# Kernel optimization log

Hardware: AMD Instinct MI355X
Metric: run time of the kernel (lower is better)

Reference implementation:

```python
import jax, jax.numpy as jnp
import numpy as np

T, B, E, H, V, L = 128, 64, 1024, 1024, 10000, 2


def setup_inputs() -> dict:
    key = jax.random.key(0)
    ks = jax.random.split(key, 10)
    k = 1.0 / np.sqrt(H)
    u = lambda kk, shape, a: jax.random.uniform(kk, shape, jnp.float32, -a, a)
    return {
        "emb_table": u(ks[0], (V, E), 0.1),
        "W_in0": u(ks[1], (H, E), k),   # first layer input weight (no bias in linear_W)
        "Wh0": u(ks[2], (H, H), k),
        "b0": u(ks[3], (H,), k),
        "W_in1": u(ks[4], (H, H), k),
        "Wh1": u(ks[5], (H, H), k),
        "b1": u(ks[6], (H,), k),
        "Wdec": u(ks[7], (V, H), 0.1),
        "bdec": jnp.zeros((V,), jnp.float32),
        "hidden": jnp.zeros((L, B, H), jnp.float32),
        "tokens": jax.random.randint(ks[8], (T, B), 0, V, jnp.int32),
    }


def reference(emb_table, W_in0, Wh0, b0, W_in1, Wh1, b1, Wdec, bdec, hidden, tokens):
    # dp_keep_prob = 1.0 -> dropout is identity
    x_emb = emb_table[tokens]  # [T, B, E]

    def step(h, x):
        # h: [L, B, H]; x: [B, E]
        h0 = jnp.tanh(x @ W_in0.T + h[0] @ Wh0.T + b0)
        h1 = jnp.tanh(h0 @ W_in1.T + h[1] @ Wh1.T + b1)
        logits_t = h1 @ Wdec.T + bdec  # [B, V]
        return jnp.stack([h0, h1]), logits_t

    h_final, logits = jax.lax.scan(step, hidden, x_emb)
    return logits, h_final  # [T, B, V], [L, B, H]
```

## Files before the change

### kernel.cpp

```cpp
#include <hip/hip_runtime.h>
#include <hip/hip_bf16.h>
#include <stdint.h>

typedef __bf16 bf16_t;
typedef __bf16 bf16x8 __attribute__((ext_vector_type(8)));
typedef __bf16 bf16x4 __attribute__((ext_vector_type(4)));
typedef float  floatx4 __attribute__((ext_vector_type(4)));

#define T_STEPS 128
#define BATCH   64
#define EDIM    1024
#define HDIM    1024
#define VOCAB   10000
#define MROWS   (T_STEPS * BATCH)
#define RNN_BLOCKS 128
#define DEC_BLOCKS 128
#define BH      (BATCH * HDIM)
#define FSTRIDE 16
#define VTILES  79
#define NUNITS  (64 * VTILES)

__device__ __forceinline__ floatx4 mfma16(bf16x8 a, bf16x8 b, floatx4 c) {
    return __builtin_amdgcn_mfma_f32_16x16x32_bf16(a, b, c, 0, 0, 0);
}

__device__ __forceinline__ void gl_lds16(const bf16_t* g, bf16_t* l) {
    __builtin_amdgcn_global_load_lds(
        (const __attribute__((address_space(1))) void*)g,
        (__attribute__((address_space(3))) void*)l, 16, 0, 0);
}

__device__ __forceinline__ void store_bf16_bypass(bf16_t* p, float v) {
    union { bf16_t b; unsigned short u; } cv;
    cv.b = (bf16_t)v;
    unsigned int d = cv.u;
    asm volatile("global_store_short %0, %1, off sc0 sc1"
                 :: "v"(p), "v"(d) : "memory");
}


__global__ void f2b_kernel(const float* __restrict__ s, bf16_t* __restrict__ d, int n) {
    int i = (blockIdx.x * blockDim.x + threadIdx.x) * 4;
    if (i < n) {
        float4 v = *(const float4*)(s + i);
        bf16x4 o;
        o.x = (bf16_t)v.x; o.y = (bf16_t)v.y; o.z = (bf16_t)v.z; o.w = (bf16_t)v.w;
        *(bf16x4*)(d + i) = o;
    }
}

__global__ void gather_kernel(const float* __restrict__ emb, const int* __restrict__ tok,
                              bf16_t* __restrict__ X) {
    int row = blockIdx.x;
    int t = tok[row];
    int e = threadIdx.x * 4;
    float4 v = *(const float4*)(emb + (size_t)t * EDIM + e);
    bf16x4 o;
    o.x = (bf16_t)v.x; o.y = (bf16_t)v.y; o.z = (bf16_t)v.z; o.w = (bf16_t)v.w;
    *(bf16x4*)(X + (size_t)row * EDIM + e) = o;
}

__global__ void init_state_kernel(const float* __restrict__ hidden,
                                  bf16_t* __restrict__ h0all, bf16_t* __restrict__ h1all,
                                  int* __restrict__ flags) {
    int i = blockIdx.x * blockDim.x + threadIdx.x;
    h0all[i] = (bf16_t)hidden[i];
    h1all[i] = (bf16_t)hidden[BATCH * HDIM + i];
    if (i < 128 * FSTRIDE) flags[i] = 0;
}


template <int OUT_BF16>
__global__ __launch_bounds__(256) void gemm_kernel(
    const bf16_t* __restrict__ A, const bf16_t* __restrict__ W,
    const float* __restrict__ bias, void* __restrict__ out,
    int M, int N, int K)
{
    const int tid  = threadIdx.x;
    const int lane = tid & 63;
    const int wave = tid >> 6;
    const int wm   = wave & 1;
    const int wn   = wave >> 1;
    const int quad = lane >> 4;
    const int l16  = lane & 15;
    const int mTile = blockIdx.y * 128;
    const int nTile = blockIdx.x * 128;

    __shared__ __align__(16) bf16_t sA[128 * 32];
    __shared__ __align__(16) bf16_t sW[128 * 32];

    const floatx4 fzero = {0.f, 0.f, 0.f, 0.f};
    floatx4 acc[4][4];
    #pragma unroll
    for (int i = 0; i < 4; ++i)
        #pragma unroll
        for (int j = 0; j < 4; ++j) acc[i][j] = fzero;

    for (int kk = 0; kk < K; kk += 32) {
        __syncthreads();
        #pragma unroll
        for (int j = 0; j < 2; ++j) {
            int c   = tid + j * 256;
            int row = c >> 2;
            int sub = c & 3;
            gl_lds16(A + (size_t)(mTile + row) * K + kk + sub * 8, sA + c * 8);
            int wrow = nTile + row;
            if (wrow >= N) wrow = N - 1;
            gl_lds16(W + (size_t)wrow * K + kk + sub * 8, sW + c * 8);
        }
        __syncthreads();
        bf16x8 af[4], wf[4];
        #pragma unroll
        for (int mi = 0; mi < 4; ++mi)
            af[mi] = *(const bf16x8*)(sA + (wm * 64 + mi * 16 + l16) * 32 + quad * 8);
        #pragma unroll
        for (int ni = 0; ni < 4; ++ni)
            wf[ni] = *(const bf16x8*)(sW + (wn * 64 + ni * 16 + l16) * 32 + quad * 8);
        #pragma unroll
        for (int mi = 0; mi < 4; ++mi)
            #pragma unroll
            for (int ni = 0; ni < 4; ++ni)
                acc[mi][ni] = mfma16(af[mi], wf[ni], acc[mi][ni]);
    }

    #pragma unroll
    for (int ni = 0; ni < 4; ++ni) {
        int col = nTile + wn * 64 + ni * 16 + l16;
        if (col < N) {
            float bv = bias[col];
            #pragma unroll
            for (int mi = 0; mi < 4; ++mi) {
                #pragma unroll
                for (int r = 0; r < 4; ++r) {
                    int row = mTile + wm * 64 + mi * 16 + quad * 4 + r;
                    float v = acc[mi][ni][r] + bv;
                    if (OUT_BF16) ((bf16_t*)out)[(size_t)row * N + col] = (bf16_t)v;
                    else          ((float*)out)[(size_t)row * N + col] = v;
                }
            }
        }
    }
}


__global__ __launch_bounds__(256, 1) void rnn_step_kernel(
    const bf16_t* __restrict__ X0,
    const bf16_t* __restrict__ Wh0b,
    const bf16_t* __restrict__ Win1b,
    const bf16_t* __restrict__ Wh1b,
    const float*  __restrict__ b1,
    const bf16_t* __restrict__ Wdecb,
    const float*  __restrict__ bdec,
    float* __restrict__ logits,
    bf16_t* __restrict__ h0all,
    bf16_t* __restrict__ h1all,
    int* __restrict__ flags)
{
    __shared__ __align__(16) char smem[65536];
    const int tid  = threadIdx.x;
    const int lane = tid & 63;
    const int wave = tid >> 6;
    const int quad = lane >> 4;
    const int l16  = lane & 15;
    int* f0 = flags;
    int* f1 = flags + 64 * FSTRIDE;
    const floatx4 fzero = {0.f, 0.f, 0.f, 0.f};

    if (blockIdx.x >= RNN_BLOCKS) {
        const int d  = blockIdx.x - RNN_BLOCKS;
        const int wm = wave & 1;
        const int wn = wave >> 1;
        bf16_t* sA = (bf16_t*)smem;
        bf16_t* sW = (bf16_t*)(smem + 8192);
        const bf16_t* Adec = h1all + BH;
        int vc = 0;
        for (int u = d; u < NUNITS; u += DEC_BLOCKS) {
            const int tp = u / VTILES;
            const int vt = u - tp * VTILES;
            const int need = 2 * tp + 2;
            if (wave == 0) {
                while (!__all(vc >= need)) {
                    if (vc < need) {
                        vc = __hip_atomic_load(&f1[lane * FSTRIDE], __ATOMIC_RELAXED,
                                               __HIP_MEMORY_SCOPE_AGENT);
                        if (vc < need) __builtin_amdgcn_s_sleep(32);
                    }
                }
            }
            __syncthreads();
            const int mTile = tp * 128;
            const int nTile = vt * 128;
            floatx4 acc[4][4];
            #pragma unroll
            for (int i = 0; i < 4; ++i)
                #pragma unroll
                for (int j = 0; j < 4; ++j) acc[i][j] = fzero;
            for (int kk = 0; kk < HDIM; kk += 32) {
                __syncthreads();
                #pragma unroll
                for (int j = 0; j < 2; ++j) {
                    int c   = tid + j * 256;
                    int row = c >> 2;
                    int sub = c & 3;
                    gl_lds16(Adec + (size_t)(mTile + row) * HDIM + kk + sub * 8, sA + c * 8);
                    int wrow = nTile + row;
                    if (wrow >= VOCAB) wrow = VOCAB - 1;
                    gl_lds16(Wdecb + (size_t)wrow * HDIM + kk + sub * 8, sW + c * 8);
                }
                __syncthreads();
                bf16x8 af[4], wf[4];
                #pragma unroll
                for (int mi = 0; mi < 4; ++mi)
                    af[mi] = *(const bf16x8*)(sA + (wm * 64 + mi * 16 + l16) * 32 + quad * 8);
                #pragma unroll
                for (int ni = 0; ni < 4; ++ni)
                    wf[ni] = *(const bf16x8*)(sW + (wn * 64 + ni * 16 + l16) * 32 + quad * 8);
                #pragma unroll
                for (int mi = 0; mi < 4; ++mi)
                    #pragma unroll
                    for (int ni = 0; ni < 4; ++ni)
                        acc[mi][ni] = mfma16(af[mi], wf[ni], acc[mi][ni]);
            }
            #pragma unroll
            for (int ni = 0; ni < 4; ++ni) {
                int col = nTile + wn * 64 + ni * 16 + l16;
                if (col < VOCAB) {
                    float bv = bdec[col];
                    #pragma unroll
                    for (int mi = 0; mi < 4; ++mi) {
                        #pragma unroll
                        for (int r = 0; r < 4; ++r) {
                            int row = mTile + wm * 64 + mi * 16 + quad * 4 + r;
                            logits[(size_t)row * VOCAB + col] = acc[mi][ni][r] + bv;
                        }
                    }
                }
            }
            __syncthreads();
        }
        return;
    }

    const bool isL1 = blockIdx.x >= 64;
    const int cb    = blockIdx.x & 63;
    const int cbase = cb * 16;
    const int colg  = cbase + l16;
    const int arow  = (wave * 16 + l16) * HDIM;
    const int orow0 = wave * 16 + quad * 4;

    {
        const bf16_t* W0 = isL1 ? Win1b : Wh0b;
        for (int c = tid; c < 2048; c += 256) {
            int kc2 = c >> 6, ln = c & 63;
            const bf16_t* src = W0 + (size_t)(cbase + (ln & 15)) * HDIM + kc2 * 32 + (ln >> 4) * 8;
            *(int4*)(smem + c * 16) = *(const int4*)src;
        }
        if (isL1) {
            for (int c = tid; c < 2048; c += 256) {
                int kc2 = c >> 6, ln = c & 63;
                const bf16_t* src = Wh1b + (size_t)(cbase + (ln & 15)) * HDIM + kc2 * 32 + (ln >> 4) * 8;
                *(int4*)(smem + 32768 + c * 16) = *(const int4*)src;
            }
        }
    }
    __syncthreads();

    if (!isL1) {
        float xr[4];
        #pragma unroll
        for (int r = 0; r < 4; ++r)
            xr[r] = (float)X0[(size_t)(orow0 + r) * HDIM + colg];
        int vc = 0;
        for (int t = 0; t < T_STEPS; ++t) {
            if (t > 0) {
                if (wave == 0) {
                    while (!__all(vc >= t)) {
                        if (vc < t) {
                            vc = __hip_atomic_load(&f0[lane * FSTRIDE], __ATOMIC_RELAXED,
                                                   __HIP_MEMORY_SCOPE_AGENT);
                            if (vc < t) __builtin_amdgcn_s_sleep(1);
                        }
                    }
                }
                __syncthreads();
            }
            const bf16_t* Ap = h0all + (size_t)t * BH;
            bf16x8 av[32];
            #pragma unroll
            for (int kc = 0; kc < 32; ++kc)
                av[kc] = *(const bf16x8*)(Ap + arow + kc * 32 + quad * 8);
            float xn[4];
            if (t + 1 < T_STEPS) {
                #pragma unroll
                for (int r = 0; r < 4; ++r)
                    xn[r] = (float)X0[((size_t)(t + 1) * BATCH + orow0 + r) * HDIM + colg];
            }
            __builtin_amdgcn_sched_barrier(0);
            floatx4 a0 = fzero, a1 = fzero;
            #pragma unroll
            for (int kc = 0; kc < 32; ++kc) {
                bf16x8 wv = *(const bf16x8*)(smem + kc * 1024 + lane * 16);
                if (kc & 1) a1 = mfma16(av[kc], wv, a1);
                else        a0 = mfma16(av[kc], wv, a0);
            }
            bf16_t* dst = h0all + (size_t)(t + 1) * BH;
            #pragma unroll
            for (int r = 0; r < 4; ++r)
                store_bf16_bypass(dst + (size_t)(orow0 + r) * HDIM + colg,
                                  tanhf(xr[r] + a0[r] + a1[r]));
            if (t + 1 < T_STEPS) {
                #pragma unroll
                for (int r = 0; r < 4; ++r) xr[r] = xn[r];
            }
            asm volatile("s_waitcnt vmcnt(0)" ::: "memory");
            __syncthreads();
            if (tid == 0)
                __hip_atomic_store(&f0[cb * FSTRIDE], t + 1, __ATOMIC_RELAXED,
                                   __HIP_MEMORY_SCOPE_AGENT);
        }
    } else {
        const float bb = b1[colg];
        int vc0 = 0, vc1 = 0;
        for (int t = 0; t < T_STEPS; ++t) {
            if (wave == 0) {
                while (!__all(vc0 >= t + 1)) {
                    if (vc0 < t + 1) {
                        vc0 = __hip_atomic_load(&f0[lane * FSTRIDE], __ATOMIC_RELAXED,
                                                __HIP_MEMORY_SCOPE_AGENT);
                        if (vc0 < t + 1) __builtin_amdgcn_s_sleep(1);
                    }
                }
            }
            __syncthreads();
            const bf16_t* A0 = h0all + (size_t)(t + 1) * BH;
            bf16x8 av0[32];
            #pragma unroll
            for (int kc = 0; kc < 32; ++kc)
                av0[kc] = *(const bf16x8*)(A0 + arow + kc * 32 + quad * 8);
            __builtin_amdgcn_sched_barrier(0);
            floatx4 aA = fzero, aB = fzero;
            #pragma unroll
            for (int kc = 0; kc < 32; ++kc) {
                bf16x8 wv1 = *(const bf16x8*)(smem + kc * 1024 + lane * 16);
                if (kc & 1) aB = mfma16(av0[kc], wv1, aB);
                else        aA = mfma16(av0[kc], wv1, aA);
            }
            if (t > 0) {
                if (wave == 0) {
                    while (!__all(vc1 >= t)) {
                        if (vc1 < t) {
                            vc1 = __hip_atomic_load(&f1[lane * FSTRIDE], __ATOMIC_RELAXED,
                                                    __HIP_MEMORY_SCOPE_AGENT);
                            if (vc1 < t) __builtin_amdgcn_s_sleep(1);
                        }
                    }
                }
                __syncthreads();
            }
            const bf16_t* A1 = h1all + (size_t)t * BH;
            bf16x8 av1[32];
            #pragma unroll
            for (int kc = 0; kc < 32; ++kc)
                av1[kc] = *(const bf16x8*)(A1 + arow + kc * 32 + quad * 8);
            __builtin_amdgcn_sched_barrier(0);
            #pragma unroll
            for (int kc = 0; kc < 32; ++kc) {
                bf16x8 wv2 = *(const bf16x8*)(smem + 32768 + kc * 1024 + lane * 16);
                if (kc & 1) aB = mfma16(av1[kc], wv2, aB);
                else        aA = mfma16(av1[kc], wv2, aA);
            }
            bf16_t* dst = h1all + (size_t)(t + 1) * BH;
            #pragma unroll
            for (int r = 0; r < 4; ++r)
                store_bf16_bypass(dst + (size_t)(orow0 + r) * HDIM + colg,
                                  tanhf(aA[r] + aB[r] + bb));
            asm volatile("s_waitcnt vmcnt(0)" ::: "memory");
            __syncthreads();
            if (tid == 0)
                __hip_atomic_store(&f1[cb * FSTRIDE], t + 1, __ATOMIC_RELAXED,
                                   __HIP_MEMORY_SCOPE_AGENT);
        }
    }
}

__global__ void finalize_kernel(const bf16_t* __restrict__ h0all,
                                const bf16_t* __restrict__ h1all,
                                float* __restrict__ out) {
    int i = blockIdx.x * blockDim.x + threadIdx.x;
    const size_t OUT0 = (size_t)MROWS * VOCAB;
    out[OUT0 + i]                = (float)h0all[(size_t)T_STEPS * BATCH * HDIM + i];
    out[OUT0 + BATCH * HDIM + i] = (float)h1all[(size_t)T_STEPS * BATCH * HDIM + i];
}


extern "C" void kernel_launch(void* const* d_in, const int* in_sizes, int n_in,
                              void* d_out, int out_size, void* d_ws, size_t ws_size,
                              hipStream_t stream) {
    (void)in_sizes; (void)n_in; (void)out_size; (void)ws_size;
    const float* emb    = (const float*)d_in[0];
    const float* W_in0  = (const float*)d_in[1];
    const float* Wh0    = (const float*)d_in[2];
    const float* b0     = (const float*)d_in[3];
    const float* W_in1  = (const float*)d_in[4];
    const float* Wh1    = (const float*)d_in[5];
    const float* b1     = (const float*)d_in[6];
    const float* Wdec   = (const float*)d_in[7];
    const float* bdec   = (const float*)d_in[8];
    const float* hidden = (const float*)d_in[9];
    const int*   tokens = (const int*)d_in[10];
    float* out = (float*)d_out;

    char* ws = (char*)d_ws;
    auto alloc = [&](size_t bytes) {
        char* p = ws; ws += (bytes + 255) & ~(size_t)255; return p;
    };
    bf16_t* Xemb  = (bf16_t*)alloc((size_t)MROWS * EDIM * 2);
    bf16_t* X0    = (bf16_t*)alloc((size_t)MROWS * HDIM * 2);
    bf16_t* Win0b = (bf16_t*)alloc((size_t)HDIM * EDIM * 2);
    bf16_t* Wh0b  = (bf16_t*)alloc((size_t)HDIM * HDIM * 2);
    bf16_t* Win1b = (bf16_t*)alloc((size_t)HDIM * HDIM * 2);
    bf16_t* Wh1b  = (bf16_t*)alloc((size_t)HDIM * HDIM * 2);
    bf16_t* Wdecb = (bf16_t*)alloc((size_t)VOCAB * HDIM * 2);
    bf16_t* h1all = (bf16_t*)alloc((size_t)(T_STEPS + 1) * BATCH * HDIM * 2);
    bf16_t* h0all = (bf16_t*)alloc((size_t)(T_STEPS + 1) * BATCH * HDIM * 2);
    int*    flags = (int*)alloc(128 * FSTRIDE * 4);

    f2b_kernel<<<dim3(HDIM * EDIM / 1024), 256, 0, stream>>>(W_in0, Win0b, HDIM * EDIM);
    f2b_kernel<<<dim3(HDIM * HDIM / 1024), 256, 0, stream>>>(Wh0,   Wh0b,  HDIM * HDIM);
    f2b_kernel<<<dim3(HDIM * HDIM / 1024), 256, 0, stream>>>(W_in1, Win1b, HDIM * HDIM);
    f2b_kernel<<<dim3(HDIM * HDIM / 1024), 256, 0, stream>>>(Wh1,   Wh1b,  HDIM * HDIM);
    f2b_kernel<<<dim3(VOCAB * HDIM / 1024), 256, 0, stream>>>(Wdec, Wdecb, VOCAB * HDIM);
    gather_kernel<<<dim3(MROWS), 256, 0, stream>>>(emb, tokens, Xemb);
    init_state_kernel<<<dim3(256), 256, 0, stream>>>(hidden, h0all, h1all, flags);

    gemm_kernel<1><<<dim3(HDIM / 128, MROWS / 128), 256, 0, stream>>>(
        Xemb, Win0b, b0, X0, MROWS, HDIM, EDIM);

    rnn_step_kernel<<<dim3(RNN_BLOCKS + DEC_BLOCKS), 256, 0, stream>>>(
        X0, Wh0b, Win1b, Wh1b, b1, Wdecb, bdec, out, h0all, h1all, flags);

    finalize_kernel<<<dim3(256), 256, 0, stream>>>(h0all, h1all, out);
}
```

Baseline: 1.489 ms.

## Fuse input projection GEMM into persistent RNN kernel with per-tile readiness flags

Merges the conversion, gather and init kernels into one setup launch and removes the separate input-projection GEMM and finalize kernels. The decoder blocks first compute the X0 = Xemb·W_in0ᵀ+b0 tiles and publish per-tile flags, which the layer-0 recurrent blocks poll before consuming each timestep pair. This lets the projection overlap the start of the recurrence. The decoder's work assignment also changes to a fixed vocab tile per block over a range of time tiles, and final hidden states are written directly from the recurrent loop. In exchange it adds flag polling on the recurrence's critical path and uneven decoder load (some blocks handle 32 time tiles, others 64).

```diff
diff --git a/kernel.cpp b/kernel.cpp
--- a/kernel.cpp
+++ b/kernel.cpp
@@ -17,8 +17,8 @@
 #define DEC_BLOCKS 128
 #define BH      (BATCH * HDIM)
 #define FSTRIDE 16
-#define VTILES  79
-#define NUNITS  (64 * VTILES)
+#define XF_OFF  (128 * FSTRIDE)
+#define OUT0    ((size_t)MROWS * VOCAB)
 
 __device__ __forceinline__ floatx4 mfma16(bf16x8 a, bf16x8 b, floatx4 c) {
     return __builtin_amdgcn_mfma_f32_16x16x32_bf16(a, b, c, 0, 0, 0);
@@ -38,120 +38,71 @@
                  :: "v"(p), "v"(d) : "memory");
 }
 
-
-__global__ void f2b_kernel(const float* __restrict__ s, bf16_t* __restrict__ d, int n) {
-    int i = (blockIdx.x * blockDim.x + threadIdx.x) * 4;
-    if (i < n) {
+__device__ __forceinline__ void wait_flag1(const int* p) {
+    while (__hip_atomic_load(p, __ATOMIC_RELAXED, __HIP_MEMORY_SCOPE_AGENT) == 0)
+        __builtin_amdgcn_s_sleep(1);
+}
+
+
+__global__ void setup_kernel(const float* __restrict__ emb,
+                             const float* __restrict__ W_in0, const float* __restrict__ Wh0,
+                             const float* __restrict__ W_in1, const float* __restrict__ Wh1,
+                             const float* __restrict__ Wdec,
+                             const float* __restrict__ hidden, const int* __restrict__ tok,
+                             bf16_t* __restrict__ Xemb,
+                             bf16_t* __restrict__ Win0b, bf16_t* __restrict__ Wh0b,
+                             bf16_t* __restrict__ Win1b, bf16_t* __restrict__ Wh1b,
+                             bf16_t* __restrict__ Wdecb,
+                             bf16_t* __restrict__ h0all, bf16_t* __restrict__ h1all,
+                             int* __restrict__ flags) {
+    const int b = blockIdx.x, tid = threadIdx.x;
+    if (b < 4096) {
+        const int which = b >> 10;
+        const float* s = which == 0 ? W_in0 : which == 1 ? Wh0 : which == 2 ? W_in1 : Wh1;
+        bf16_t*      d = which == 0 ? Win0b : which == 1 ? Wh0b : which == 2 ? Win1b : Wh1b;
+        int i = ((b & 1023) * 256 + tid) * 4;
         float4 v = *(const float4*)(s + i);
-        bf16x4 o;
-        o.x = (bf16_t)v.x; o.y = (bf16_t)v.y; o.z = (bf16_t)v.z; o.w = (bf16_t)v.w;
+        bf16x4 o; o.x = (bf16_t)v.x; o.y = (bf16_t)v.y; o.z = (bf16_t)v.z; o.w = (bf16_t)v.w;
         *(bf16x4*)(d + i) = o;
+    } else if (b < 14096) {
+        int i = ((b - 4096) * 256 + tid) * 4;
+        float4 v = *(const float4*)(Wdec + i);
+        bf16x4 o; o.x = (bf16_t)v.x; o.y = (bf16_t)v.y; o.z = (bf16_t)v.z; o.w = (bf16_t)v.w;
+        *(bf16x4*)(Wdecb + i) = o;
+    } else if (b < 22288) {
+        int row = b - 14096;
+        int t = tok[row];
+        int e = tid * 4;
+        float4 v = *(const float4*)(emb + (size_t)t * EDIM + e);
+        bf16x4 o; o.x = (bf16_t)v.x; o.y = (bf16_t)v.y; o.z = (bf16_t)v.z; o.w = (bf16_t)v.w;
+        *(bf16x4*)(Xemb + (size_t)row * EDIM + e) = o;
+    } else {
+        int i = ((b - 22288) * 256 + tid) * 4;
+        float4 v0 = *(const float4*)(hidden + i);
+        float4 v1 = *(const float4*)(hidden + BH + i);
+        bf16x4 o0, o1;
+        o0.x = (bf16_t)v0.x; o0.y = (bf16_t)v0.y; o0.z = (bf16_t)v0.z; o0.w = (bf16_t)v0.w;
+        o1.x = (bf16_t)v1.x; o1.y = (bf16_t)v1.y; o1.z = (bf16_t)v1.z; o1.w = (bf16_t)v1.w;
+        *(bf16x4*)(h0all + i) = o0;
+        *(bf16x4*)(h1all + i) = o1;
+        if (b == 22288)
+            for (int j = tid; j < XF_OFF + 512; j += 256) flags[j] = 0;
     }
 }
 
-__global__ void gather_kernel(const float* __restrict__ emb, const int* __restrict__ tok,
-                              bf16_t* __restrict__ X) {
-    int row = blockIdx.x;
-    int t = tok[row];
-    int e = threadIdx.x * 4;
-    float4 v = *(const float4*)(emb + (size_t)t * EDIM + e);
-    bf16x4 o;
-    o.x = (bf16_t)v.x; o.y = (bf16_t)v.y; o.z = (bf16_t)v.z; o.w = (bf16_t)v.w;
-    *(bf16x4*)(X + (size_t)row * EDIM + e) = o;
-}
-
-__global__ void init_state_kernel(const float* __restrict__ hidden,
-                                  bf16_t* __restrict__ h0all, bf16_t* __restrict__ h1all,
-                                  int* __restrict__ flags) {
-    int i = blockIdx.x * blockDim.x + threadIdx.x;
-    h0all[i] = (bf16_t)hidden[i];
-    h1all[i] = (bf16_t)hidden[BATCH * HDIM + i];
-    if (i < 128 * FSTRIDE) flags[i] = 0;
-}
-
-
-template <int OUT_BF16>
-__global__ __launch_bounds__(256) void gemm_kernel(
-    const bf16_t* __restrict__ A, const bf16_t* __restrict__ W,
-    const float* __restrict__ bias, void* __restrict__ out,
-    int M, int N, int K)
-{
-    const int tid  = threadIdx.x;
-    const int lane = tid & 63;
-    const int wave = tid >> 6;
-    const int wm   = wave & 1;
-    const int wn   = wave >> 1;
-    const int quad = lane >> 4;
-    const int l16  = lane & 15;
-    const int mTile = blockIdx.y * 128;
-    const int nTile = blockIdx.x * 128;
-
-    __shared__ __align__(16) bf16_t sA[128 * 32];
-    __shared__ __align__(16) bf16_t sW[128 * 32];
-
-    const floatx4 fzero = {0.f, 0.f, 0.f, 0.f};
-    floatx4 acc[4][4];
-    #pragma unroll
-    for (int i = 0; i < 4; ++i)
-        #pragma unroll
-        for (int j = 0; j < 4; ++j) acc[i][j] = fzero;
-
-    for (int kk = 0; kk < K; kk += 32) {
-        __syncthreads();
-        #pragma unroll
-        for (int j = 0; j < 2; ++j) {
-            int c   = tid + j * 256;
-            int row = c >> 2;
-            int sub = c & 3;
-            gl_lds16(A + (size_t)(mTile + row) * K + kk + sub * 8, sA + c * 8);
-            int wrow = nTile + row;
-            if (wrow >= N) wrow = N - 1;
-            gl_lds16(W + (size_t)wrow * K + kk + sub * 8, sW + c * 8);
-        }
-        __syncthreads();
-        bf16x8 af[4], wf[4];
-        #pragma unroll
-        for (int mi = 0; mi < 4; ++mi)
-            af[mi] = *(const bf16x8*)(sA + (wm * 64 + mi * 16 + l16) * 32 + quad * 8);
-        #pragma unroll
-        for (int ni = 0; ni < 4; ++ni)
-            wf[ni] = *(const bf16x8*)(sW + (wn * 64 + ni * 16 + l16) * 32 + quad * 8);
-        #pragma unroll
-        for (int mi = 0; mi < 4; ++mi)
-            #pragma unroll
-            for (int ni = 0; ni < 4; ++ni)
-                acc[mi][ni] = mfma16(af[mi], wf[ni], acc[mi][ni]);
-    }
-
-    #pragma unroll
-    for (int ni = 0; ni < 4; ++ni) {
-        int col = nTile + wn * 64 + ni * 16 + l16;
-        if (col < N) {
-            float bv = bias[col];
-            #pragma unroll
-            for (int mi = 0; mi < 4; ++mi) {
-                #pragma unroll
-                for (int r = 0; r < 4; ++r) {
-                    int row = mTile + wm * 64 + mi * 16 + quad * 4 + r;
-                    float v = acc[mi][ni][r] + bv;
-                    if (OUT_BF16) ((bf16_t*)out)[(size_t)row * N + col] = (bf16_t)v;
-                    else          ((float*)out)[(size_t)row * N + col] = v;
-                }
-            }
-        }
-    }
-}
-
-
-__global__ __launch_bounds__(256, 1) void rnn_step_kernel(
-    const bf16_t* __restrict__ X0,
+
+__global__ __launch_bounds__(256, 1) void fused_kernel(
+    bf16_t* __restrict__ X0,
+    const bf16_t* __restrict__ Xemb,
+    const bf16_t* __restrict__ Win0b,
+    const float*  __restrict__ b0,
     const bf16_t* __restrict__ Wh0b,
     const bf16_t* __restrict__ Win1b,
     const bf16_t* __restrict__ Wh1b,
     const float*  __restrict__ b1,
     const bf16_t* __restrict__ Wdecb,
     const float*  __restrict__ bdec,
-    float* __restrict__ logits,
+    float* __restrict__ out,
     bf16_t* __restrict__ h0all,
     bf16_t* __restrict__ h1all,
     int* __restrict__ flags)
@@ -164,6 +115,7 @@
     const int l16  = lane & 15;
     int* f0 = flags;
     int* f1 = flags + 64 * FSTRIDE;
+    int* xf = flags + XF_OFF;
     const floatx4 fzero = {0.f, 0.f, 0.f, 0.f};
 
     if (blockIdx.x >= RNN_BLOCKS) {
@@ -172,11 +124,67 @@
         const int wn = wave >> 1;
         bf16_t* sA = (bf16_t*)smem;
         bf16_t* sW = (bf16_t*)(smem + 8192);
+
+        for (int u = d; u < 512; u += DEC_BLOCKS) {
+            const int mTile = (u >> 3) * 128;
+            const int nTile = (u & 7) * 128;
+            floatx4 acc[4][4];
+            #pragma unroll
+            for (int i = 0; i < 4; ++i)
+                #pragma unroll
+                for (int j = 0; j < 4; ++j) acc[i][j] = fzero;
+            for (int kk = 0; kk < EDIM; kk += 32) {
+                __syncthreads();
+                #pragma unroll
+                for (int j = 0; j < 2; ++j) {
+                    int c   = tid + j * 256;
+                    int row = c >> 2;
+                    int sub = c & 3;
+                    gl_lds16(Xemb  + (size_t)(mTile + row) * EDIM + kk + sub * 8, sA + c * 8);
+                    gl_lds16(Win0b + (size_t)(nTile + row) * EDIM + kk + sub * 8, sW + c * 8);
+                }
+                __syncthreads();
+                bf16x8 af[4], wf[4];
+                #pragma unroll
+                for (int mi = 0; mi < 4; ++mi)
+                    af[mi] = *(const bf16x8*)(sA + (wm * 64 + mi * 16 + l16) * 32 + quad * 8);
+                #pragma unroll
+                for (int ni = 0; ni < 4; ++ni)
+                    wf[ni] = *(const bf16x8*)(sW + (wn * 64 + ni * 16 + l16) * 32 + quad * 8);
+                #pragma unroll
+                for (int mi = 0; mi < 4; ++mi)
+                    #pragma unroll
+                    for (int ni = 0; ni < 4; ++ni)
+                        acc[mi][ni] = mfma16(af[mi], wf[ni], acc[mi][ni]);
+            }
+            #pragma unroll
+            for (int ni = 0; ni < 4; ++ni) {
+                int col = nTile + wn * 64 + ni * 16 + l16;
+                float bv = b0[col];
+                #pragma unroll
+                for (int mi = 0; mi < 4; ++mi) {
+                    #pragma unroll
+                    for (int r = 0; r < 4; ++r) {
+                        int row = mTile + wm * 64 + mi * 16 + quad * 4 + r;
+                        store_bf16_bypass(X0 + (size_t)row * HDIM + col,
+                                          acc[mi][ni][r] + bv);
+                    }
+                }
+            }
+            asm volatile("s_waitcnt vmcnt(0)" ::: "memory");
+            __syncthreads();
+            if (tid == 0)
+                __hip_atomic_store(&xf[u], 1, __ATOMIC_RELAXED, __HIP_MEMORY_SCOPE_AGENT);
+            __syncthreads();
+        }
+
+        int vt, tp0, tpN;
+        if (d < 79) { vt = d;      tp0 = 0;  tpN = (d < 49) ? 32 : 64; }
+        else        { vt = d - 79; tp0 = 32; tpN = 64; }
         const bf16_t* Adec = h1all + BH;
+        const int nTile = vt * 128;
         int vc = 0;
-        for (int u = d; u < NUNITS; u += DEC_BLOCKS) {
-            const int tp = u / VTILES;
-            const int vt = u - tp * VTILES;
+        for (int tp = tp0; tp < tpN; ++tp) {
             const int need = 2 * tp + 2;
             if (wave == 0) {
                 while (!__all(vc >= need)) {
@@ -189,7 +197,6 @@
             }
             __syncthreads();
             const int mTile = tp * 128;
-            const int nTile = vt * 128;
             floatx4 acc[4][4];
             #pragma unroll
             for (int i = 0; i < 4; ++i)
@@ -231,7 +238,7 @@
                         #pragma unroll
                         for (int r = 0; r < 4; ++r) {
                             int row = mTile + wm * 64 + mi * 16 + quad * 4 + r;
-                            logits[(size_t)row * VOCAB + col] = acc[mi][ni][r] + bv;
+                            out[(size_t)row * VOCAB + col] = acc[mi][ni][r] + bv;
                         }
                     }
                 }
@@ -266,10 +273,13 @@
     __syncthreads();
 
     if (!isL1) {
+        const int nt0 = cb >> 3;
+        wait_flag1(&xf[nt0]);
         float xr[4];
         #pragma unroll
         for (int r = 0; r < 4; ++r)
             xr[r] = (float)X0[(size_t)(orow0 + r) * HDIM + colg];
+        int xdone = 0;
         int vc = 0;
         for (int t = 0; t < T_STEPS; ++t) {
             if (t > 0) {
@@ -291,6 +301,8 @@
                 av[kc] = *(const bf16x8*)(Ap + arow + kc * 32 + quad * 8);
             float xn[4];
             if (t + 1 < T_STEPS) {
+                int m = (t + 1) >> 1;
+                if (m > xdone) { wait_flag1(&xf[m * 8 + nt0]); xdone = m; }
                 #pragma unroll
                 for (int r = 0; r < 4; ++r)
                     xn[r] = (float)X0[((size_t)(t + 1) * BATCH + orow0 + r) * HDIM + colg];
@@ -305,9 +317,12 @@
             }
             bf16_t* dst = h0all + (size_t)(t + 1) * BH;
             #pragma unroll
-            for (int r = 0; r < 4; ++r)
-                store_bf16_bypass(dst + (size_t)(orow0 + r) * HDIM + colg,
-                                  tanhf(xr[r] + a0[r] + a1[r]));
+            for (int r = 0; r < 4; ++r) {
+                float hv = tanhf(xr[r] + a0[r] + a1[r]);
+                store_bf16_bypass(dst + (size_t)(orow0 + r) * HDIM + colg, hv);
+                if (t == T_STEPS - 1)
+                    out[OUT0 + (size_t)(orow0 + r) * HDIM + colg] = hv;
+            }
             if (t + 1 < T_STEPS) {
                 #pragma unroll
                 for (int r = 0; r < 4; ++r) xr[r] = xn[r];
@@ -371,9 +386,12 @@
             }
             bf16_t* dst = h1all + (size_t)(t + 1) * BH;
             #pragma unroll
-            for (int r = 0; r < 4; ++r)
-                store_bf16_bypass(dst + (size_t)(orow0 + r) * HDIM + colg,
-                                  tanhf(aA[r] + aB[r] + bb));
+            for (int r = 0; r < 4; ++r) {
+                float hv = tanhf(aA[r] + aB[r] + bb);
+                store_bf16_bypass(dst + (size_t)(orow0 + r) * HDIM + colg, hv);
+                if (t == T_STEPS - 1)
+                    out[OUT0 + BH + (size_t)(orow0 + r) * HDIM + colg] = hv;
+            }
             asm volatile("s_waitcnt vmcnt(0)" ::: "memory");
             __syncthreads();
             if (tid == 0)
@@ -381,15 +399,6 @@
                                    __HIP_MEMORY_SCOPE_AGENT);
         }
     }
-}
-
-__global__ void finalize_kernel(const bf16_t* __restrict__ h0all,
-                                const bf16_t* __restrict__ h1all,
-                                float* __restrict__ out) {
-    int i = blockIdx.x * blockDim.x + threadIdx.x;
-    const size_t OUT0 = (size_t)MROWS * VOCAB;
-    out[OUT0 + i]                = (float)h0all[(size_t)T_STEPS * BATCH * HDIM + i];
-    out[OUT0 + BATCH * HDIM + i] = (float)h1all[(size_t)T_STEPS * BATCH * HDIM + i];
 }
 
 
@@ -423,21 +432,13 @@
     bf16_t* Wdecb = (bf16_t*)alloc((size_t)VOCAB * HDIM * 2);
     bf16_t* h1all = (bf16_t*)alloc((size_t)(T_STEPS + 1) * BATCH * HDIM * 2);
     bf16_t* h0all = (bf16_t*)alloc((size_t)(T_STEPS + 1) * BATCH * HDIM * 2);
-    int*    flags = (int*)alloc(128 * FSTRIDE * 4);
-
-    f2b_kernel<<<dim3(HDIM * EDIM / 1024), 256, 0, stream>>>(W_in0, Win0b, HDIM * EDIM);
-    f2b_kernel<<<dim3(HDIM * HDIM / 1024), 256, 0, stream>>>(Wh0,   Wh0b,  HDIM * HDIM);
-    f2b_kernel<<<dim3(HDIM * HDIM / 1024), 256, 0, stream>>>(W_in1, Win1b, HDIM * HDIM);
-    f2b_kernel<<<dim3(HDIM * HDIM / 1024), 256, 0, stream>>>(Wh1,   Wh1b,  HDIM * HDIM);
-    f2b_kernel<<<dim3(VOCAB * HDIM / 1024), 256, 0, stream>>>(Wdec, Wdecb, VOCAB * HDIM);
-    gather_kernel<<<dim3(MROWS), 256, 0, stream>>>(emb, tokens, Xemb);
-    init_state_kernel<<<dim3(256), 256, 0, stream>>>(hidden, h0all, h1all, flags);
-
-    gemm_kernel<1><<<dim3(HDIM / 128, MROWS / 128), 256, 0, stream>>>(
-        Xemb, Win0b, b0, X0, MROWS, HDIM, EDIM);
-
-    rnn_step_kernel<<<dim3(RNN_BLOCKS + DEC_BLOCKS), 256, 0, stream>>>(
-        X0, Wh0b, Win1b, Wh1b, b1, Wdecb, bdec, out, h0all, h1all, flags);
-
-    finalize_kernel<<<dim3(256), 256, 0, stream>>>(h0all, h1all, out);
-}
+    int*    flags = (int*)alloc((XF_OFF + 512) * 4);
+
+    setup_kernel<<<dim3(22352), 256, 0, stream>>>(
+        emb, W_in0, Wh0, W_in1, Wh1, Wdec, hidden, tokens,
+        Xemb, Win0b, Wh0b, Win1b, Wh1b, Wdecb, h0all, h1all, flags);
+
+    fused_kernel<<<dim3(RNN_BLOCKS + DEC_BLOCKS), 256, 0, stream>>>(
+        X0, Xemb, Win0b, b0, Wh0b, Win1b, Wh1b, b1, Wdecb, bdec,
+        out, h0all, h1all, flags);
+}
```

Measured after the change: 1.645 ms. 1.1x slower.
